# Optimization experiments

Hardware: AMD Instinct MI355X
Metric: run time of the kernel (lower is better)

The kernel has to match this reference:

```python
import jax, jax.numpy as jnp
from jax import lax
import numpy as np
import math

B, H, W = 4, 64, 64
D_MODEL, D_STATE, D_CONV, EXPAND, K = 96, 16, 3, 2, 4
D_INNER = EXPAND * D_MODEL          # 192
DT_RANK = math.ceil(D_MODEL / 16)   # 6


def setup_inputs() -> dict:
    key = jax.random.key(0)
    ks = jax.random.split(key, 12)
    s = 0.02
    rgb = jax.random.normal(ks[0], (B, H, W, D_MODEL), jnp.float32)
    t = jax.random.normal(ks[1], (B, H, W, D_MODEL), jnp.float32)
    in_proj1_w = jax.random.normal(ks[2], (2 * D_INNER, D_MODEL), jnp.float32) * s
    in_proj2_w = jax.random.normal(ks[3], (2 * D_INNER, D_MODEL), jnp.float32) * s
    conv1_w = jax.random.normal(ks[4], (D_INNER, 1, D_CONV, D_CONV), jnp.float32) * s
    conv1_b = jnp.zeros((D_INNER,), jnp.float32)
    conv2_w = jax.random.normal(ks[5], (D_INNER, 1, D_CONV, D_CONV), jnp.float32) * s
    conv2_b = jnp.zeros((D_INNER,), jnp.float32)
    x_proj_weight = jax.random.normal(ks[6], (K, DT_RANK + 2 * D_STATE, D_INNER), jnp.float32) * s
    lim = DT_RANK ** -0.5
    dt_projs_weight = jax.random.uniform(ks[7], (K, D_INNER, DT_RANK), jnp.float32, -lim, lim)
    dt = jnp.exp(jax.random.uniform(ks[8], (K, D_INNER), jnp.float32)
                 * (math.log(0.1) - math.log(0.001)) + math.log(0.001))
    dt = jnp.clip(dt, 1e-4, None)
    dt_projs_bias = dt + jnp.log(-jnp.expm1(-dt))  # inverse softplus
    A_logs = jnp.tile(jnp.log(jnp.arange(1, D_STATE + 1, dtype=jnp.float32))[None], (K * D_INNER, 1))
    Ds = jnp.ones((K * D_INNER,), jnp.float32)
    norm1_w = jnp.ones((D_INNER,), jnp.float32); norm1_b = jnp.zeros((D_INNER,), jnp.float32)
    norm2_w = jnp.ones((D_INNER,), jnp.float32); norm2_b = jnp.zeros((D_INNER,), jnp.float32)
    out_proj1_w = jax.random.normal(ks[9], (D_MODEL, D_INNER), jnp.float32) * s
    out_proj2_w = jax.random.normal(ks[10], (D_MODEL, D_INNER), jnp.float32) * s
    return dict(rgb=rgb, t=t, in_proj1_w=in_proj1_w, in_proj2_w=in_proj2_w,
                conv1_w=conv1_w, conv1_b=conv1_b, conv2_w=conv2_w, conv2_b=conv2_b,
                x_proj_weight=x_proj_weight, dt_projs_weight=dt_projs_weight,
                dt_projs_bias=dt_projs_bias, A_logs=A_logs, Ds=Ds,
                norm1_w=norm1_w, norm1_b=norm1_b, norm2_w=norm2_w, norm2_b=norm2_b,
                out_proj1_w=out_proj1_w, out_proj2_w=out_proj2_w)


def _dwconv(x, w, b):
    # x: (B, C, H, W), depthwise 3x3, padding=1
    y = lax.conv_general_dilated(x, w, (1, 1), 'SAME',
                                 feature_group_count=x.shape[1],
                                 dimension_numbers=('NCHW', 'OIHW', 'NCHW'))
    return y + b[None, :, None, None]


def _ln(x, w, b, eps=1e-5):
    m = x.mean(-1, keepdims=True)
    v = ((x - m) ** 2).mean(-1, keepdims=True)
    return (x - m) / jnp.sqrt(v + eps) * w + b


def _cross_scan(x):
    # x: (B, C, H, W) -> (B, 4, C, L): row-major, col-major, and their reverses
    Bz, C, Hh, Ww = x.shape
    L = Hh * Ww
    xr = x.reshape(Bz, C, L)
    xt = x.transpose(0, 1, 3, 2).reshape(Bz, C, L)
    xh = jnp.stack([xr, xt], 1)                        # (B,2,C,L)
    return jnp.concatenate([xh, jnp.flip(xh, -1)], 1)  # (B,4,C,L)


def _cross_merge(y, Hh, Ww):
    # y: (B, 4, C, L) -> (B, C, L); undo scan directions then sum
    Bz, _, C, L = y.shape
    inv = jnp.flip(y[:, 2:4], -1)                      # (B,2,C,L)
    wh = y[:, 1].reshape(Bz, C, Ww, Hh).transpose(0, 1, 3, 2).reshape(Bz, C, L)
    invwh = inv[:, 1].reshape(Bz, C, Ww, Hh).transpose(0, 1, 3, 2).reshape(Bz, C, L)
    return y[:, 0] + inv[:, 0] + wh + invwh


def _selective_scan(u, delta, A, Bs, Cs, Ds, delta_bias):
    # u, delta: (B, K, C, L2); A: (K, C, N); Bs, Cs: (B, K, N, L2); Ds: (K, C)
    Bz, Kk, C, L2 = u.shape
    N = A.shape[-1]
    delta = jax.nn.softplus(delta + delta_bias[None, :, :, None])

    def step(h, inp):
        d_l, u_l, B_l, C_l = inp               # (B,K,C),(B,K,C),(B,K,N),(B,K,N)
        dA = jnp.exp(d_l[..., None] * A[None])            # (B,K,C,N)
        dBu = (d_l * u_l)[..., None] * B_l[:, :, None, :]  # (B,K,C,N)
        h = h * dA + dBu
        y = jnp.einsum('bkcn,bkn->bkc', h, C_l)
        return h, y

    h0 = jnp.zeros((Bz, Kk, C, N), u.dtype)
    seq = (delta.transpose(3, 0, 1, 2), u.transpose(3, 0, 1, 2),
           Bs.transpose(3, 0, 1, 2), Cs.transpose(3, 0, 1, 2))
    _, ys = lax.scan(step, h0, seq)            # (L2, B, K, C)
    y = ys.transpose(1, 2, 3, 0)               # (B, K, C, L2)
    return y + u * Ds[None, :, :, None]


def _forward_core(x1, x2, x_proj_weight, dt_projs_weight, dt_projs_bias, A_logs, Ds):
    # x1, x2: (B, C, H, W)
    Bz, C, Hh, Ww = x1.shape
    L = Hh * Ww
    rgb4 = _cross_scan(x1)                     # (B,4,C,L)
    t4 = _cross_scan(x2)
    # interleave modalities along sequence: [..., rgb_i, t_i, ...] length 2L
    xs = jnp.stack([rgb4, t4], -1).reshape(Bz, K, C, 2 * L)
    x_dbl = jnp.einsum('bkdl,kcd->bkcl', xs, x_proj_weight)
    dts, Bm, Cm = jnp.split(x_dbl, [DT_RANK, DT_RANK + D_STATE], axis=2)
    dts = jnp.einsum('bkrl,kdr->bkdl', dts, dt_projs_weight)   # (B,K,C,2L)
    As = -jnp.exp(A_logs.astype(jnp.float32)).reshape(K, C, D_STATE)
    y = _selective_scan(xs, dts, As, Bm, Cm, Ds.reshape(K, C), dt_projs_bias)
    y = y.reshape(Bz, K, C, L, 2)
    y_rgb = _cross_merge(y[..., 0], Hh, Ww)    # (B,C,L)
    y_t = _cross_merge(y[..., 1], Hh, Ww)
    return y_rgb, y_t


def reference(rgb, t, in_proj1_w, in_proj2_w, conv1_w, conv1_b, conv2_w, conv2_b,
              x_proj_weight, dt_projs_weight, dt_projs_bias, A_logs, Ds,
              norm1_w, norm1_b, norm2_w, norm2_b, out_proj1_w, out_proj2_w):
    Bz, Hh, Ww, _ = rgb.shape
    x1, z1 = jnp.split(rgb @ in_proj1_w.T, 2, -1)
    x2, z2 = jnp.split(t @ in_proj2_w.T, 2, -1)
    x1 = jax.nn.silu(_dwconv(x1.transpose(0, 3, 1, 2), conv1_w, conv1_b))
    x2 = jax.nn.silu(_dwconv(x2.transpose(0, 3, 1, 2), conv2_w, conv2_b))
    y_rgb, y_t = _forward_core(x1, x2, x_proj_weight, dt_projs_weight,
                               dt_projs_bias, A_logs, Ds)
    y_rgb = _ln(y_rgb.transpose(0, 2, 1).reshape(Bz, Hh, Ww, D_INNER), norm1_w, norm1_b)
    y_t = _ln(y_t.transpose(0, 2, 1).reshape(Bz, Hh, Ww, D_INNER), norm2_w, norm2_b)
    out1 = (y_rgb * jax.nn.silu(z1)) @ out_proj1_w.T
    out2 = (y_t * jax.nn.silu(z2)) @ out_proj2_w.T
    return out1, out2
```

## Files before the change

### kernel.cpp

```cpp
#include <hip/hip_runtime.h>
#include <math.h>

#define BB   4
#define LL   4096
#define L2T  8192
#define DM   96
#define CI   192
#define KD   4
#define NN   16
#define RR   6
#define BKT  16
#define SS   128
#define TT   64
#define DBLS 40

#define OFF_XPRE1 0
#define OFF_XPRE2 3145728
#define OFF_Z1    6291456
#define OFF_Z2    9437184
#define OFF_X1C   12582912
#define OFF_X2C   15728640
#define OFF_DBL   18874368
#define OFF_MERG  24117248
#define OFF_DSUM  30408704

__global__ __launch_bounds__(256)
void k_inproj(const float* __restrict__ rgb, const float* __restrict__ tin,
              const float* __restrict__ w1, const float* __restrict__ w2,
              float* __restrict__ xp1, float* __restrict__ xp2,
              float* __restrict__ zz1, float* __restrict__ zz2) {
  int mb = blockIdx.x;
  int nb = blockIdx.y;
  int m  = blockIdx.z;
  const float* in = m ? tin : rgb;
  const float* w  = (m ? w2 : w1) + nb * 96 * DM;
  __shared__ float As[64][100];
  __shared__ float Ws[96][98];
  int t = threadIdx.x;
  const float4* asrc = (const float4*)(in + (size_t)mb * 64 * DM);
  for (int i = t; i < 1536; i += 256) {
    int r = i / 24, kk = (i % 24) * 4;
    *(float4*)&As[r][kk] = asrc[i];
  }
  const float2* wsrc = (const float2*)w;
  for (int i = t; i < 4608; i += 256) {
    int r = i / 48, kk = (i % 48) * 2;
    *(float2*)&Ws[r][kk] = wsrc[i];
  }
  __syncthreads();
  int tc = t & 15, tr = t >> 4;
  float acc[4][6] = {};
  for (int k = 0; k < 96; k += 2) {
    float2 a[4], b[6];
#pragma unroll
    for (int i = 0; i < 4; i++) a[i] = *(const float2*)&As[tr * 4 + i][k];
#pragma unroll
    for (int j = 0; j < 6; j++) b[j] = *(const float2*)&Ws[tc * 6 + j][k];
#pragma unroll
    for (int i = 0; i < 4; i++)
#pragma unroll
      for (int j = 0; j < 6; j++) {
        acc[i][j] = fmaf(a[i].x, b[j].x, acc[i][j]);
        acc[i][j] = fmaf(a[i].y, b[j].y, acc[i][j]);
      }
  }
  float* dst = (nb < 2) ? (m ? xp2 : xp1) : (m ? zz2 : zz1);
  int colbase = (nb & 1) * 96 + tc * 6;
#pragma unroll
  for (int i = 0; i < 4; i++) {
    size_t bl = (size_t)mb * 64 + tr * 4 + i;
#pragma unroll
    for (int j = 0; j < 6; j++)
      dst[bl * CI + colbase + j] = acc[i][j];
  }
}

__global__ __launch_bounds__(256)
void k_conv(const float* __restrict__ xp1, const float* __restrict__ xp2,
            const float* __restrict__ c1w, const float* __restrict__ c1b,
            const float* __restrict__ c2w, const float* __restrict__ c2b,
            float* __restrict__ o1, float* __restrict__ o2) {
  int m = blockIdx.y;
  const float* in = m ? xp2 : xp1;
  const float* cw = m ? c2w : c1w;
  const float* cb = m ? c2b : c1b;
  float* out = m ? o2 : o1;
  int idx = blockIdx.x * 256 + threadIdx.x;
  int c = idx % CI;
  int bl = idx / CI;
  int b = bl / LL, l = bl % LL;
  int hh = l >> 6, ww = l & 63;
  float a = cb[c];
#pragma unroll
  for (int di = 0; di < 3; di++) {
    int h2 = hh + di - 1;
    if ((unsigned)h2 >= 64u) continue;
#pragma unroll
    for (int dj = 0; dj < 3; dj++) {
      int w2 = ww + dj - 1;
      if ((unsigned)w2 >= 64u) continue;
      a = fmaf(in[(b * LL + h2 * 64 + w2) * CI + c], cw[c * 9 + di * 3 + dj], a);
    }
  }
  out[idx] = a / (1.f + __expf(-a));
}

__global__ __launch_bounds__(256)
void k_dbl(const float* __restrict__ x1c, const float* __restrict__ x2c,
           const float* __restrict__ wx, float* __restrict__ dbl) {
  int pt = blockIdx.x;
  int bk = blockIdx.y;
  int b = bk >> 2, k = bk & 3;
  __shared__ float As[64][100];
  __shared__ float Ws[40][100];
  int t = threadIdx.x;
  int tc = t & 7, tr = t >> 3;
  float acc[2][5] = {};
  for (int kc = 0; kc < 2; kc++) {
    if (kc) __syncthreads();
    for (int i = t; i < 1536; i += 256) {
      int r = i / 24, kk = (i % 24) * 4;
      int l2 = pt * 64 + r;
      int mm = l2 & 1, l = l2 >> 1;
      int lt = (k >= 2) ? (LL - 1 - l) : l;
      int sp = (k & 1) ? (((lt & 63) << 6) | (lt >> 6)) : lt;
      const float* src = (mm ? x2c : x1c) + ((size_t)(b * LL + sp)) * CI + kc * 96;
      *(float4*)&As[r][kk] = *(const float4*)(src + kk);
    }
    for (int i = t; i < 960; i += 256) {
      int r = i / 24, kk = (i % 24) * 4;
      float4 v;
      if (r < 38) v = *(const float4*)&wx[(size_t)(k * 38 + r) * CI + kc * 96 + kk];
      else        v = float4{0.f, 0.f, 0.f, 0.f};
      *(float4*)&Ws[r][kk] = v;
    }
    __syncthreads();
    for (int kk2 = 0; kk2 < 96; kk2 += 2) {
      float2 a[2], bv[5];
#pragma unroll
      for (int i = 0; i < 2; i++) a[i] = *(const float2*)&As[tr * 2 + i][kk2];
#pragma unroll
      for (int j = 0; j < 5; j++) bv[j] = *(const float2*)&Ws[tc * 5 + j][kk2];
#pragma unroll
      for (int i = 0; i < 2; i++)
#pragma unroll
        for (int j = 0; j < 5; j++) {
          acc[i][j] = fmaf(a[i].x, bv[j].x, acc[i][j]);
          acc[i][j] = fmaf(a[i].y, bv[j].y, acc[i][j]);
        }
    }
  }
#pragma unroll
  for (int i = 0; i < 2; i++) {
    size_t row = (size_t)bk * L2T + pt * 64 + tr * 2 + i;
#pragma unroll
    for (int j = 0; j < 5; j++) {
      int cc = tc * 5 + j;
      if (cc < 38) dbl[row * DBLS + cc] = acc[i][j];
    }
  }
}

template<int PASS>
__global__ __launch_bounds__(192)
void k_scan(const float* __restrict__ x1c, const float* __restrict__ x2c,
            const float* __restrict__ dbl,
            const float* __restrict__ dtw, const float* __restrict__ dtb,
            const float* __restrict__ alogs, const float* __restrict__ dsv,
            float* __restrict__ hend, float* __restrict__ dsum,
            const float* __restrict__ hin, float* __restrict__ merged) {
  int bid = blockIdx.x;
  int s  = bid & (SS - 1);
  int bk = bid >> 7;
  int b = bk >> 2, kdir = bk & 3;
  int c = threadIdx.x;
  int kc = kdir * CI + c;

  float w2r0 = dtw[kc * RR + 0], w2r1 = dtw[kc * RR + 1], w2r2 = dtw[kc * RR + 2];
  float w2r3 = dtw[kc * RR + 3], w2r4 = dtw[kc * RR + 4], w2r5 = dtw[kc * RR + 5];
  float bias = dtb[kc];
  float Dv   = (PASS == 2) ? dsv[kc] : 0.f;
  float Areg[NN];
#pragma unroll
  for (int n = 0; n < NN; n++) Areg[n] = -__expf(alogs[kc * NN + n]);
  float A1 = Areg[0];
  int ok = 1;
#pragma unroll
  for (int n = 1; n < NN; n++) {
    float want = A1 * (float)(n + 1);
    if (!(fabsf(Areg[n] - want) <= fabsf(want) * 1e-3f + 1e-6f)) ok = 0;
  }
  const bool structured = (__all(ok) != 0);

  float h[NN];
  if (PASS == 2) {
    int base = ((s * BKT + bk) * CI + c) * NN;
#pragma unroll
    for (int n = 0; n < NN; n++) h[n] = hin[base + n];
  } else {
#pragma unroll
    for (int n = 0; n < NN; n++) h[n] = 0.f;
  }
  float dacc = 0.f;

  const float4* dp4 = (const float4*)(dbl + (size_t)(bk * L2T + s * TT) * DBLS);
  const float* u1b = x1c + (size_t)b * LL * CI + c;
  const float* u2b = x2c + (size_t)b * LL * CI + c;

  auto spmap = [&](int l) -> int {
    int lt = (kdir >= 2) ? (LL - 1 - l) : l;
    return (kdir & 1) ? (((lt & 63) << 6) | (lt >> 6)) : lt;
  };

  auto loadrow = [&](float4* Q, int t) {
    const float4* r4 = dp4 + t * 10;
    Q[0] = r4[0]; Q[1] = r4[1]; Q[2] = r4[2];
    Q[3] = r4[3]; Q[4] = r4[4]; Q[5] = r4[5];
    if (PASS == 2) { Q[6] = r4[6]; Q[7] = r4[7]; Q[8] = r4[8]; Q[9] = r4[9]; }
  };

#define DG(Q, i) ((i & 3) == 0 ? Q[(i) >> 2].x : (i & 3) == 1 ? Q[(i) >> 2].y : (i & 3) == 2 ? Q[(i) >> 2].z : Q[(i) >> 2].w)

  auto step = [&](const float4* Q, float u, float& y) {
    float x = bias;
    x = fmaf(DG(Q, 0), w2r0, x); x = fmaf(DG(Q, 1), w2r1, x); x = fmaf(DG(Q, 2), w2r2, x);
    x = fmaf(DG(Q, 3), w2r3, x); x = fmaf(DG(Q, 4), w2r4, x); x = fmaf(DG(Q, 5), w2r5, x);
    float delta = (x > 15.f) ? x : __logf(1.f + __expf(x));
    float du = delta * u;
    float y0 = 0.f, y1 = 0.f, y2 = 0.f, y3 = 0.f;
    if (structured) {
      float r  = __expf(delta * A1);
      float r2 = r * r, r3 = r2 * r, r4 = r2 * r2;
      float r6 = r4 * r2, r8 = r4 * r4;
      float pw[NN];
      pw[0] = r;       pw[1] = r2;      pw[2] = r3;      pw[3] = r4;
      pw[4] = r4 * r;  pw[5] = r6;      pw[6] = r4 * r3; pw[7] = r8;
      pw[8] = r8 * r;  pw[9] = r8 * r2; pw[10] = r8 * r3; pw[11] = r8 * r4;
      pw[12] = r8 * pw[4]; pw[13] = r8 * r6; pw[14] = r8 * pw[6]; pw[15] = r8 * r8;
#pragma unroll
      for (int n = 0; n < NN; n++) {
        h[n] = fmaf(h[n], pw[n], du * DG(Q, 6 + n));
        if (PASS == 2) {
          float* yp = (n & 2) ? ((n & 1) ? &y3 : &y2) : ((n & 1) ? &y1 : &y0);
          *yp = fmaf(h[n], DG(Q, 22 + n), *yp);
        }
      }
    } else {
#pragma unroll
      for (int n = 0; n < NN; n++) {
        float dA = __expf(delta * Areg[n]);
        h[n] = fmaf(h[n], dA, du * DG(Q, 6 + n));
        if (PASS == 2) {
          float* yp = (n & 2) ? ((n & 1) ? &y3 : &y2) : ((n & 1) ? &y1 : &y0);
          *yp = fmaf(h[n], DG(Q, 22 + n), *yp);
        }
      }
    }
    if (PASS == 1) dacc += delta;
    else y = fmaf(u, Dv, (y0 + y1) + (y2 + y3));
  };

  const int NP = TT / 2;
  int l0 = (s * TT) >> 1;
  float4 qA[10], qB[10];
  int spC = spmap(l0);
  float u1C = u1b[(size_t)spC * CI];
  float u2C = u2b[(size_t)spC * CI];
  int spN = spmap(l0 + 1);
  float u1N = u1b[(size_t)spN * CI];
  float u2N = u2b[(size_t)spN * CI];
  int spN2 = spmap(l0 + 2);
  float u1N2 = u1b[(size_t)spN2 * CI];
  float u2N2 = u2b[(size_t)spN2 * CI];
  loadrow(qA, 0);
#pragma unroll 1
  for (int t = 0; t < TT; t += 2) {
    int p = t >> 1;
    loadrow(qB, t + 1);
    int spN3 = 0; float u1N3 = 0.f, u2N3 = 0.f;
    if (p + 3 < NP) {
      spN3 = spmap(l0 + p + 3);
      u1N3 = u1b[(size_t)spN3 * CI];
      u2N3 = u2b[(size_t)spN3 * CI];
    }
    float ya, yb;
    step(qA, u1C, ya);
    if (t + 2 < TT) loadrow(qA, t + 2);
    step(qB, u2C, yb);
    if (PASS == 2) {
      float* mrow = merged + (size_t)(b * LL + spC) * (2 * CI) + c;
      atomicAdd(mrow, ya);
      atomicAdd(mrow + CI, yb);
    }
    spC = spN;  u1C = u1N;  u2C = u2N;
    spN = spN2; u1N = u1N2; u2N = u2N2;
    spN2 = spN3; u1N2 = u1N3; u2N2 = u2N3;
  }
#undef DG

  if (PASS == 1) {
    int base = ((s * BKT + bk) * CI + c) * NN;
#pragma unroll
    for (int n = 0; n < NN; n++) hend[base + n] = h[n];
    dsum[(s * BKT + bk) * CI + c] = dacc;
  }
}

__global__ __launch_bounds__(256)
void k_prop(const float* __restrict__ hend, const float* __restrict__ dsum,
            const float* __restrict__ alogs, float* __restrict__ hin) {
  int idx = blockIdx.x * 256 + threadIdx.x;
  int n = idx & 15;
  int rest = idx >> 4;
  int c = rest % CI;
  int bk = rest / CI;
  int k = bk & 3;
  float A = -__expf(alogs[(k * CI + c) * NN + n]);
  float h = 0.f;
  for (int s = 0; s < SS; s++) {
    int cell = (s * BKT + bk) * CI + c;
    hin[cell * NN + n] = h;
    float ap = __expf(A * dsum[cell]);
    h = h * ap + hend[cell * NN + n];
  }
}

__global__ __launch_bounds__(192)
void k_lngate(float* __restrict__ merged,
              const float* __restrict__ z1, const float* __restrict__ z2,
              const float* __restrict__ n1w, const float* __restrict__ n1b,
              const float* __restrict__ n2w, const float* __restrict__ n2b) {
  int bid = blockIdx.x;
  int m = bid & 1;
  int bl = bid >> 1;
  int c = threadIdx.x;
  float v = merged[(size_t)bid * CI + c];
  float s1 = v, s2 = v * v;
  for (int o = 32; o > 0; o >>= 1) {
    s1 += __shfl_xor(s1, o);
    s2 += __shfl_xor(s2, o);
  }
  __shared__ float red[2][3];
  int wv = threadIdx.x >> 6, ln = threadIdx.x & 63;
  if (ln == 0) { red[0][wv] = s1; red[1][wv] = s2; }
  __syncthreads();
  float S1 = red[0][0] + red[0][1] + red[0][2];
  float S2 = red[1][0] + red[1][1] + red[1][2];
  float mean = S1 * (1.f / CI);
  float var = S2 * (1.f / CI) - mean * mean;
  float rstd = rsqrtf(var + 1e-5f);
  const float* nw = m ? n2w : n1w;
  const float* nb = m ? n2b : n1b;
  float vn = (v - mean) * rstd * nw[c] + nb[c];
  float z = (m ? z2 : z1)[(size_t)bl * CI + c];
  float g = vn * (z / (1.f + __expf(-z)));
  merged[(size_t)bid * CI + c] = g;
}

__global__ __launch_bounds__(256)
void k_outproj(const float* __restrict__ g,
               const float* __restrict__ w1, const float* __restrict__ w2,
               float* __restrict__ out) {
  int mb = blockIdx.x;
  int m  = blockIdx.y;
  const float* w = m ? w2 : w1;
  __shared__ float As[64][100];
  __shared__ float Ws[96][98];
  int t = threadIdx.x;
  int tc = t & 15, tr = t >> 4;
  float acc[4][6] = {};
  for (int kc = 0; kc < 2; kc++) {
    if (kc) __syncthreads();
    for (int i = t; i < 1536; i += 256) {
      int r = i / 24, kk = (i % 24) * 4;
      *(float4*)&As[r][kk] =
          *(const float4*)&g[((size_t)(mb * 64 + r) * 2 + m) * CI + kc * 96 + kk];
    }
    for (int i = t; i < 4608; i += 256) {
      int r = i / 48, kk = (i % 48) * 2;
      *(float2*)&Ws[r][kk] = *(const float2*)&w[(size_t)r * CI + kc * 96 + kk];
    }
    __syncthreads();
    for (int k = 0; k < 96; k += 2) {
      float2 a[4], b[6];
#pragma unroll
      for (int i = 0; i < 4; i++) a[i] = *(const float2*)&As[tr * 4 + i][k];
#pragma unroll
      for (int j = 0; j < 6; j++) b[j] = *(const float2*)&Ws[tc * 6 + j][k];
#pragma unroll
      for (int i = 0; i < 4; i++)
#pragma unroll
        for (int j = 0; j < 6; j++) {
          acc[i][j] = fmaf(a[i].x, b[j].x, acc[i][j]);
          acc[i][j] = fmaf(a[i].y, b[j].y, acc[i][j]);
        }
    }
  }
  float* outp = out + (size_t)m * (BB * LL * DM);
#pragma unroll
  for (int i = 0; i < 4; i++) {
    size_t bl = (size_t)mb * 64 + tr * 4 + i;
#pragma unroll
    for (int j = 0; j < 6; j++)
      outp[bl * DM + tc * 6 + j] = acc[i][j];
  }
}

extern "C" void kernel_launch(void* const* d_in, const int* in_sizes, int n_in,
                              void* d_out, int out_size, void* d_ws, size_t ws_size,
                              hipStream_t stream) {
  const float* rgb = (const float*)d_in[0];
  const float* tin = (const float*)d_in[1];
  const float* ip1 = (const float*)d_in[2];
  const float* ip2 = (const float*)d_in[3];
  const float* c1w = (const float*)d_in[4];
  const float* c1b = (const float*)d_in[5];
  const float* c2w = (const float*)d_in[6];
  const float* c2b = (const float*)d_in[7];
  const float* wx  = (const float*)d_in[8];
  const float* dtw = (const float*)d_in[9];
  const float* dtb = (const float*)d_in[10];
  const float* alg = (const float*)d_in[11];
  const float* Dsp = (const float*)d_in[12];
  const float* n1w = (const float*)d_in[13];
  const float* n1b = (const float*)d_in[14];
  const float* n2w = (const float*)d_in[15];
  const float* n2b = (const float*)d_in[16];
  const float* op1 = (const float*)d_in[17];
  const float* op2 = (const float*)d_in[18];

  float* ws = (float*)d_ws;
  float* xp1 = ws + OFF_XPRE1;
  float* xp2 = ws + OFF_XPRE2;
  float* z1  = ws + OFF_Z1;
  float* z2  = ws + OFF_Z2;
  float* x1c = ws + OFF_X1C;
  float* x2c = ws + OFF_X2C;
  float* dbl = ws + OFF_DBL;
  float* mg  = ws + OFF_MERG;
  float* dsm = ws + OFF_DSUM;
  float* he  = ws + OFF_MERG;
  float* hi  = ws + OFF_XPRE1;
  float* out = (float*)d_out;

  k_inproj<<<dim3(256, 4, 2), 256, 0, stream>>>(rgb, tin, ip1, ip2, xp1, xp2, z1, z2);
  k_conv<<<dim3(12288, 2), 256, 0, stream>>>(xp1, xp2, c1w, c1b, c2w, c2b, x1c, x2c);
  k_dbl<<<dim3(128, 16), 256, 0, stream>>>(x1c, x2c, wx, dbl);
  k_scan<1><<<SS * BKT, 192, 0, stream>>>(x1c, x2c, dbl, dtw, dtb, alg, Dsp, he, dsm, hi, mg);
  k_prop<<<192, 256, 0, stream>>>(he, dsm, alg, hi);
  hipMemsetAsync(mg, 0, (size_t)6291456 * sizeof(float), stream);
  k_scan<2><<<SS * BKT, 192, 0, stream>>>(x1c, x2c, dbl, dtw, dtb, alg, Dsp, he, dsm, hi, mg);
  k_lngate<<<BB * LL * 2, 192, 0, stream>>>(mg, z1, z2, n1w, n1b, n2w, n2b);
  k_outproj<<<dim3(256, 2), 256, 0, stream>>>(mg, op1, op2, out);
}
```

Measured before the change: 428.7 us.

## Share x tiles across reversed scan directions; prefetch prop loads; warp-per-row LN gate

k_dbl now loads each spatial tile once and computes the forward direction and its reversed counterpart together, writing the reversed result to mirrored rows. This halves the activation loads into shared memory and doubles the work per block, at the cost of more registers and shared memory and half as many blocks. k_prop software-prefetches the next segment's state and decay sum so the serial recurrence does not stall on each load. k_lngate switches from one 192-thread block per row with a shared-memory reduction to one wave per row, eight rows per wave, using only shuffle reductions.

```diff
diff --git a/kernel.cpp b/kernel.cpp
--- a/kernel.cpp
+++ b/kernel.cpp
@@ -109,54 +109,67 @@
 void k_dbl(const float* __restrict__ x1c, const float* __restrict__ x2c,
            const float* __restrict__ wx, float* __restrict__ dbl) {
   int pt = blockIdx.x;
-  int bk = blockIdx.y;
-  int b = bk >> 2, k = bk & 3;
+  int pk = blockIdx.y;
+  int b = pk >> 1, kp = pk & 1;
+  int klo = kp, khi = kp + 2;
   __shared__ float As[64][100];
-  __shared__ float Ws[40][100];
+  __shared__ float Ws[2][40][100];
   int t = threadIdx.x;
   int tc = t & 7, tr = t >> 3;
-  float acc[2][5] = {};
+  float acc[2][2][5] = {};
   for (int kc = 0; kc < 2; kc++) {
     if (kc) __syncthreads();
     for (int i = t; i < 1536; i += 256) {
       int r = i / 24, kk = (i % 24) * 4;
-      int l2 = pt * 64 + r;
-      int mm = l2 & 1, l = l2 >> 1;
-      int lt = (k >= 2) ? (LL - 1 - l) : l;
-      int sp = (k & 1) ? (((lt & 63) << 6) | (lt >> 6)) : lt;
+      int l = pt * 32 + (r >> 1);
+      int mm = r & 1;
+      int sp = kp ? (((l & 63) << 6) | (l >> 6)) : l;
       const float* src = (mm ? x2c : x1c) + ((size_t)(b * LL + sp)) * CI + kc * 96;
       *(float4*)&As[r][kk] = *(const float4*)(src + kk);
     }
-    for (int i = t; i < 960; i += 256) {
-      int r = i / 24, kk = (i % 24) * 4;
+    for (int i = t; i < 1920; i += 256) {
+      int d = i / 960;
+      int r = (i % 960) / 24, kk = (i % 24) * 4;
+      int kd = d ? khi : klo;
       float4 v;
-      if (r < 38) v = *(const float4*)&wx[(size_t)(k * 38 + r) * CI + kc * 96 + kk];
+      if (r < 38) v = *(const float4*)&wx[(size_t)(kd * 38 + r) * CI + kc * 96 + kk];
       else        v = float4{0.f, 0.f, 0.f, 0.f};
-      *(float4*)&Ws[r][kk] = v;
+      *(float4*)&Ws[d][r][kk] = v;
     }
     __syncthreads();
     for (int kk2 = 0; kk2 < 96; kk2 += 2) {
-      float2 a[2], bv[5];
+      float2 a[2], bv0[5], bv1[5];
 #pragma unroll
       for (int i = 0; i < 2; i++) a[i] = *(const float2*)&As[tr * 2 + i][kk2];
 #pragma unroll
-      for (int j = 0; j < 5; j++) bv[j] = *(const float2*)&Ws[tc * 5 + j][kk2];
+      for (int j = 0; j < 5; j++) {
+        bv0[j] = *(const float2*)&Ws[0][tc * 5 + j][kk2];
+        bv1[j] = *(const float2*)&Ws[1][tc * 5 + j][kk2];
+      }
 #pragma unroll
       for (int i = 0; i < 2; i++)
 #pragma unroll
         for (int j = 0; j < 5; j++) {
-          acc[i][j] = fmaf(a[i].x, bv[j].x, acc[i][j]);
-          acc[i][j] = fmaf(a[i].y, bv[j].y, acc[i][j]);
+          acc[0][i][j] = fmaf(a[i].x, bv0[j].x, acc[0][i][j]);
+          acc[0][i][j] = fmaf(a[i].y, bv0[j].y, acc[0][i][j]);
+          acc[1][i][j] = fmaf(a[i].x, bv1[j].x, acc[1][i][j]);
+          acc[1][i][j] = fmaf(a[i].y, bv1[j].y, acc[1][i][j]);
         }
     }
   }
 #pragma unroll
   for (int i = 0; i < 2; i++) {
-    size_t row = (size_t)bk * L2T + pt * 64 + tr * 2 + i;
+    int r = tr * 2 + i;
+    size_t rowlo = (size_t)(b * 4 + klo) * L2T + pt * 64 + r;
+    int l2p = L2T - pt * 64 - 2 * (r >> 1) - 2 + (r & 1);
+    size_t rowhi = (size_t)(b * 4 + khi) * L2T + l2p;
 #pragma unroll
     for (int j = 0; j < 5; j++) {
       int cc = tc * 5 + j;
-      if (cc < 38) dbl[row * DBLS + cc] = acc[i][j];
+      if (cc < 38) {
+        dbl[rowlo * DBLS + cc] = acc[0][i][j];
+        dbl[rowhi * DBLS + cc] = acc[1][i][j];
+      }
     }
   }
 }
@@ -317,44 +330,60 @@
   int k = bk & 3;
   float A = -__expf(alogs[(k * CI + c) * NN + n]);
   float h = 0.f;
+  int cell0 = bk * CI + c;
+  float heC = hend[(size_t)cell0 * NN + n];
+  float dsC = dsum[cell0];
+#pragma unroll 1
   for (int s = 0; s < SS; s++) {
-    int cell = (s * BKT + bk) * CI + c;
-    hin[cell * NN + n] = h;
-    float ap = __expf(A * dsum[cell]);
-    h = h * ap + hend[cell * NN + n];
-  }
-}
-
-__global__ __launch_bounds__(192)
+    float heN = 0.f, dsN = 0.f;
+    if (s + 1 < SS) {
+      int cellN = (s + 1) * BKT * CI + cell0;
+      heN = hend[(size_t)cellN * NN + n];
+      dsN = dsum[cellN];
+    }
+    int cell = s * BKT * CI + cell0;
+    hin[(size_t)cell * NN + n] = h;
+    h = h * __expf(A * dsC) + heC;
+    heC = heN; dsC = dsN;
+  }
+}
+
+__global__ __launch_bounds__(256)
 void k_lngate(float* __restrict__ merged,
               const float* __restrict__ z1, const float* __restrict__ z2,
               const float* __restrict__ n1w, const float* __restrict__ n1b,
               const float* __restrict__ n2w, const float* __restrict__ n2b) {
-  int bid = blockIdx.x;
-  int m = bid & 1;
-  int bl = bid >> 1;
-  int c = threadIdx.x;
-  float v = merged[(size_t)bid * CI + c];
-  float s1 = v, s2 = v * v;
-  for (int o = 32; o > 0; o >>= 1) {
-    s1 += __shfl_xor(s1, o);
-    s2 += __shfl_xor(s2, o);
-  }
-  __shared__ float red[2][3];
-  int wv = threadIdx.x >> 6, ln = threadIdx.x & 63;
-  if (ln == 0) { red[0][wv] = s1; red[1][wv] = s2; }
-  __syncthreads();
-  float S1 = red[0][0] + red[0][1] + red[0][2];
-  float S2 = red[1][0] + red[1][1] + red[1][2];
-  float mean = S1 * (1.f / CI);
-  float var = S2 * (1.f / CI) - mean * mean;
-  float rstd = rsqrtf(var + 1e-5f);
-  const float* nw = m ? n2w : n1w;
-  const float* nb = m ? n2b : n1b;
-  float vn = (v - mean) * rstd * nw[c] + nb[c];
-  float z = (m ? z2 : z1)[(size_t)bl * CI + c];
-  float g = vn * (z / (1.f + __expf(-z)));
-  merged[(size_t)bid * CI + c] = g;
+  int w = threadIdx.x >> 6, lane = threadIdx.x & 63;
+  int rowbase = (blockIdx.x * 4 + w) * 8;
+#pragma unroll 1
+  for (int rr = 0; rr < 8; rr++) {
+    int row = rowbase + rr;
+    int m = row & 1, blpos = row >> 1;
+    const float* gr = merged + (size_t)row * CI;
+    float v0 = gr[lane], v1 = gr[lane + 64], v2 = gr[lane + 128];
+    float s1 = v0 + v1 + v2;
+    float s2 = v0 * v0 + v1 * v1 + v2 * v2;
+#pragma unroll
+    for (int o = 32; o > 0; o >>= 1) {
+      s1 += __shfl_xor(s1, o);
+      s2 += __shfl_xor(s2, o);
+    }
+    float mean = s1 * (1.f / CI);
+    float var = s2 * (1.f / CI) - mean * mean;
+    float rstd = rsqrtf(var + 1e-5f);
+    const float* nw = m ? n2w : n1w;
+    const float* nb = m ? n2b : n1b;
+    const float* zr = (m ? z2 : z1) + (size_t)blpos * CI;
+    float* go = merged + (size_t)row * CI;
+#pragma unroll
+    for (int e = 0; e < 3; e++) {
+      int cc = lane + e * 64;
+      float v = e == 0 ? v0 : (e == 1 ? v1 : v2);
+      float vn = (v - mean) * rstd * nw[cc] + nb[cc];
+      float z = zr[cc];
+      go[cc] = vn * (z / (1.f + __expf(-z)));
+    }
+  }
 }
 
 __global__ __launch_bounds__(256)
@@ -445,11 +474,11 @@
 
   k_inproj<<<dim3(256, 4, 2), 256, 0, stream>>>(rgb, tin, ip1, ip2, xp1, xp2, z1, z2);
   k_conv<<<dim3(12288, 2), 256, 0, stream>>>(xp1, xp2, c1w, c1b, c2w, c2b, x1c, x2c);
-  k_dbl<<<dim3(128, 16), 256, 0, stream>>>(x1c, x2c, wx, dbl);
+  k_dbl<<<dim3(128, 8), 256, 0, stream>>>(x1c, x2c, wx, dbl);
   k_scan<1><<<SS * BKT, 192, 0, stream>>>(x1c, x2c, dbl, dtw, dtb, alg, Dsp, he, dsm, hi, mg);
   k_prop<<<192, 256, 0, stream>>>(he, dsm, alg, hi);
   hipMemsetAsync(mg, 0, (size_t)6291456 * sizeof(float), stream);
   k_scan<2><<<SS * BKT, 192, 0, stream>>>(x1c, x2c, dbl, dtw, dtb, alg, Dsp, he, dsm, hi, mg);
-  k_lngate<<<BB * LL * 2, 192, 0, stream>>>(mg, z1, z2, n1w, n1b, n2w, n2b);
+  k_lngate<<<1024, 256, 0, stream>>>(mg, z1, z2, n1w, n1b, n2w, n2b);
   k_outproj<<<dim3(256, 2), 256, 0, stream>>>(mg, op1, op2, out);
 }
```

After: 445.7 us. +4.0%, slower.
